# Kernel tuning notes

Measured on AMD Instinct MI355X. Metric: run time of the kernel, lower is better.

Reference implementation:

```python
import jax, jax.numpy as jnp
import numpy as np

WEIGHT = 1e-7
SIGMA_RGB = 15.0
SCALE = 0.5


def _nearest_resize(x, oh, ow):
    # PyTorch F.interpolate mode='nearest': src_idx = floor(dst * in/out)
    n, c, h, w = x.shape
    yi = (jnp.arange(oh) * (h / oh)).astype(jnp.int32)
    xi = (jnp.arange(ow) * (w / ow)).astype(jnp.int32)
    return x[:, :, yi][:, :, :, xi]


def _bilinear_resize(x, oh, ow):
    # PyTorch bilinear, align_corners=False: src = max((i+0.5)*in/out - 0.5, 0)
    n, k, h, w = x.shape

    def idx(o, s):
        src = jnp.maximum((jnp.arange(o, dtype=jnp.float32) + 0.5) * (s / o) - 0.5, 0.0)
        lo = jnp.floor(src).astype(jnp.int32)
        hi = jnp.minimum(lo + 1, s - 1)
        return lo, hi, src - lo

    ylo, yhi, fy = idx(oh, h)
    xlo, xhi, fx = idx(ow, w)
    top = x[:, :, ylo][:, :, :, xlo] * (1.0 - fx) + x[:, :, ylo][:, :, :, xhi] * fx
    bot = x[:, :, yhi][:, :, :, xlo] * (1.0 - fx) + x[:, :, yhi][:, :, :, xhi] * fx
    return top * (1.0 - fy)[:, None] + bot * fy[:, None]


def _bilateral_AS(feat, seg):
    # feat: [P,3] color features / sigma_rgb; seg: [K,P]
    # exact Gaussian color bilateral filter (what the permutohedral lattice approximates)
    sq = jnp.sum(feat * feat, axis=-1)                      # [P]
    d2 = sq[:, None] + sq[None, :] - 2.0 * (feat @ feat.T)  # [P,P]
    Kmat = jnp.exp(-0.5 * jnp.maximum(d2, 0.0))             # [P,P], symmetric
    return seg @ Kmat                                        # [K,P]


def setup_inputs() -> dict:
    key = jax.random.key(0)
    k1, k2 = jax.random.split(key)
    images = jax.random.uniform(k1, (4, 3, 128, 128), dtype=jnp.float32) * 255.0
    logits = jax.random.normal(k2, (4, 21, 128, 128), dtype=jnp.float32)
    segmentations = jax.nn.softmax(logits, axis=1)
    return {"images": images, "segmentations": segmentations}


def reference(images, segmentations):
    n, c, h, w = images.shape
    oh, ow = int(h * SCALE), int(w * SCALE)
    simg = _nearest_resize(images, oh, ow)            # [N,3,oh,ow]
    sseg = _bilinear_resize(segmentations, oh, ow)    # [N,K,oh,ow]
    P = oh * ow
    feats = simg.reshape(n, c, P).transpose(0, 2, 1) / SIGMA_RGB  # [N,P,3]
    segs = sseg.reshape(n, sseg.shape[1], P)                      # [N,K,P]
    AS = jax.vmap(_bilateral_AS)(feats, segs)                     # [N,K,P]
    loss = -jnp.sum(segs * AS) / jnp.float32(n)
    return (WEIGHT * loss).reshape(1)
```

## Files before the change

### kernel.cpp

```cpp
#include <hip/hip_runtime.h>


#define N_BATCH 4
#define IH 128
#define IW 128
#define P 4096
#define KC 21

using short8   = __attribute__((ext_vector_type(8))) short;
using floatx16 = __attribute__((ext_vector_type(16))) float;

static constexpr float INV_SIGMA = 1.0f / 15.0f;
static constexpr float LOG2E     = 1.4426950408889634f;
static constexpr float OUT_SCALE = -1e-7f / 4.0f;

#define ZP_OFF   0
#define ARGA_OFF 64
#define ARGB_OFF (ARGA_OFF + N_BATCH * P * 32)
#define SEG_OFF  (ARGB_OFF + N_BATCH * P * 32)
#define PART_OFF (SEG_OFF + N_BATCH * P * 48)

#define NFEAT (N_BATCH * P)
#define NSEG2 (N_BATCH * KC * P / 2)

#define CHUNKS 16
#define NBLOCKS (CHUNKS * 16 * N_BATCH)

__device__ __forceinline__ ushort f2bf(float x) {
    unsigned u = __builtin_bit_cast(unsigned, x);
    unsigned r = (u + 0x7FFFu + ((u >> 16) & 1u)) >> 16;
    return (ushort)r;
}
__device__ __forceinline__ float bf2f(ushort h) {
    return __builtin_bit_cast(float, (unsigned)h << 16);
}

__global__ void crf_prep(const float* __restrict__ img,
                         const float* __restrict__ seg,
                         char* __restrict__ wsb)
{
    int t = blockIdx.x * blockDim.x + threadIdx.x;
    if (t < NFEAT) {
        if (t < 16) ((float*)(wsb + ZP_OFF))[t] = 0.0f;

        int n = t >> 12;
        int p = t & (P - 1);
        int y = p >> 6, x = p & 63;

        const float* ib = img + (size_t)n * 3 * IH * IW + (size_t)(2 * y) * IW + 2 * x;
        float f0 = ib[0] * INV_SIGMA;
        float f1 = ib[IH * IW] * INV_SIGMA;
        float f2 = ib[2 * IH * IW] * INV_SIGMA;
        float h = 0.5f * (f0 * f0 + f1 * f1 + f2 * f2);

        float fa0 = f0 * LOG2E, fa1 = f1 * LOG2E, fa2 = f2 * LOG2E;
        ushort ah0 = f2bf(fa0), ah1 = f2bf(fa1), ah2 = f2bf(fa2);
        ushort al0 = f2bf(fa0 - bf2f(ah0));
        ushort al1 = f2bf(fa1 - bf2f(ah1));
        ushort al2 = f2bf(fa2 - bf2f(ah2));
        float nhL = -h * LOG2E;
        ushort nhh = f2bf(nhL), nhl = f2bf(nhL - bf2f(nhh));
        ushort bh0 = f2bf(f0), bh1 = f2bf(f1), bh2 = f2bf(f2);
        ushort bl0 = f2bf(f0 - bf2f(bh0));
        ushort bl1 = f2bf(f1 - bf2f(bh1));
        ushort bl2 = f2bf(f2 - bf2f(bh2));
        float hL = h * LOG2E;
        ushort hbh = f2bf(hL), hbl = f2bf(hL - bf2f(hbh));

        const ushort ONE = 0x3F80, NEG1 = 0xBF80;
        ushort rA[16] = {ah0, ah1, ah2, ah0, ah1, ah2, al0, al1, al2, al0, al1, al2,
                         nhh, nhl, NEG1, NEG1};
        ushort rB[16] = {bh0, bh1, bh2, bl0, bl1, bl2, bh0, bh1, bh2, bl0, bl1, bl2,
                         ONE, ONE, hbh, hbl};

        short8 vA0, vA1, vB0, vB1;
#pragma unroll
        for (int j = 0; j < 8; ++j) {
            vA0[j] = (short)rA[j];     vA1[j] = (short)rA[8 + j];
            vB0[j] = (short)rB[j];     vB1[j] = (short)rB[8 + j];
        }
        short8* dA = (short8*)(wsb + ARGA_OFF + (size_t)t * 32);
        dA[0] = vA0; dA[1] = vA1;
        short8* dB = (short8*)(wsb + ARGB_OFF + (size_t)t * 32);
        dB[0] = vB0; dB[1] = vB1;

        char* sp = wsb + SEG_OFF + (size_t)t * 48;
        *(ushort*)(sp + 42) = 0;
        *(uint*)(sp + 44) = 0;
    } else if (t < NFEAT + NSEG2) {
        int u = t - NFEAT;
        int pp = (u & 2047) * 2;
        int nk = u >> 11;
        int n = nk / 21;
        int k = nk - n * 21;
        int y = pp >> 6, x0 = pp & 63;

        const float* r0 = seg + (size_t)nk * IH * IW + (size_t)(2 * y) * IW + 2 * x0;
        float4 a = *(const float4*)r0;
        float4 b = *(const float4*)(r0 + IW);
        float v0 = 0.25f * ((a.x + a.y) + (b.x + b.y));
        float v1 = 0.25f * ((a.z + a.w) + (b.z + b.w));
        char* d = wsb + SEG_OFF + (size_t)(n * P + pp) * 48 + k * 2;
        *(ushort*)d = f2bf(v0);
        *(ushort*)(d + 48) = f2bf(v1);
    }
}

__global__ __launch_bounds__(256, 4) void crf_pair(char* __restrict__ wsb)
{
    const int n    = blockIdx.z;
    const int sp   = blockIdx.y;
    const int c    = blockIdx.x;
    const int wave = threadIdx.x >> 6;
    const int lane = threadIdx.x & 63;
    const int l32  = lane & 31;
    const int l5   = lane >> 5;

    const char* argA = wsb + ARGA_OFF + (size_t)n * P * 32;
    const char* argB = wsb + ARGB_OFF + (size_t)n * P * 32;
    const char* segT = wsb + SEG_OFF  + (size_t)n * P * 48;
    const char* zp   = wsb + ZP_OFF;

    const char* bBa = argB + l32 * 32 + l5 * 16;
    const char* bBs = segT + l32 * 48 + l5 * 16;
    const int maskH = l5 ? 0 : ~0;
    const char* bBh = l5 ? zp : (segT + l32 * 48 + 32);

    const floatx16 zc = {0.f,0.f,0.f,0.f,0.f,0.f,0.f,0.f,
                         0.f,0.f,0.f,0.f,0.f,0.f,0.f,0.f};

    short8 afA, afL, afH;

    float m0=0.f, m1=0.f, m2=0.f, m3=0.f;
    float d0=0.f, d1=0.f, d2=0.f, d3=0.f;

    auto jobM = [&](short8 ba, short8 bl, short8 bh) {
        floatx16 ar = __builtin_amdgcn_mfma_f32_32x32x16_bf16(afA, ba, zc, 0, 0, 0);
        floatx16 g  = __builtin_amdgcn_mfma_f32_32x32x16_bf16(afL, bl, zc, 0, 0, 0);
        g = __builtin_amdgcn_mfma_f32_32x32x16_bf16(afH, bh, g, 0, 0, 0);
#pragma unroll
        for (int r = 0; r < 16; ++r) {
            float t = __builtin_amdgcn_exp2f(ar[r]) * g[r];
            if ((r & 3) == 0) m0 += t;
            else if ((r & 3) == 1) m1 += t;
            else if ((r & 3) == 2) m2 += t;
            else m3 += t;
        }
    };
    auto jobD = [&](short8 ba, short8 bl, short8 bh) {
        floatx16 ar = __builtin_amdgcn_mfma_f32_32x32x16_bf16(afA, ba, zc, 0, 0, 0);
        floatx16 g  = __builtin_amdgcn_mfma_f32_32x32x16_bf16(afL, bl, zc, 0, 0, 0);
        g = __builtin_amdgcn_mfma_f32_32x32x16_bf16(afH, bh, g, 0, 0, 0);
#pragma unroll
        for (int r = 0; r < 16; ++r) {
            float t = __builtin_amdgcn_exp2f(ar[r]) * g[r];
            if ((r & 3) == 0) d0 += t;
            else if ((r & 3) == 1) d1 += t;
            else if ((r & 3) == 2) d2 += t;
            else d3 += t;
        }
    };

    auto load_A = [&](int ti) {
        int rr = ti * 32 + l32;
        afA = *(const short8*)(argA + rr * 32 + l5 * 16);
        afL = *(const short8*)(segT + rr * 48 + l5 * 16);
        afH = l5 ? *(const short8*)zp : *(const short8*)(segT + rr * 48 + 32);
    };

    auto run_main = [&](int jbase, int cnt) {
        if (cnt <= c) return;
        int nj = (cnt - c + CHUNKS - 1) / CHUNKS;
        int j0 = jbase + c;
        int oA0 = j0 * 1024, oS0 = j0 * 1536;
        int oA1 = oA0 + CHUNKS * 1024, oS1 = oS0 + CHUNKS * 1536;
        short8 a0 = *(const short8*)(bBa + oA0);
        short8 l0 = *(const short8*)(bBs + oS0);
        short8 h0 = *(const short8*)(bBh + (oS0 & maskH));
        short8 a1 = a0, l1 = l0, h1 = h0;
        if (nj > 1) {
            a1 = *(const short8*)(bBa + oA1);
            l1 = *(const short8*)(bBs + oS1);
            h1 = *(const short8*)(bBh + (oS1 & maskH));
        }
        for (int t = 0; t < nj; t += 2) {
            jobM(a0, l0, h0);
            if (t + 2 < nj) {
                oA0 += 2 * CHUNKS * 1024; oS0 += 2 * CHUNKS * 1536;
                a0 = *(const short8*)(bBa + oA0);
                l0 = *(const short8*)(bBs + oS0);
                h0 = *(const short8*)(bBh + (oS0 & maskH));
            }
            if (t + 1 < nj) {
                jobM(a1, l1, h1);
                if (t + 3 < nj) {
                    oA1 += 2 * CHUNKS * 1024; oS1 += 2 * CHUNKS * 1536;
                    a1 = *(const short8*)(bBa + oA1);
                    l1 = *(const short8*)(bBs + oS1);
                    h1 = *(const short8*)(bBh + (oS1 & maskH));
                }
            }
        }
    };

    auto run_edge = [&](int s) {
        for (int jj = wave; jj < 4; ++jj) {
            int j = 4 * s + jj;
            int oA = j * 1024, oS = j * 1536;
            short8 ba = *(const short8*)(bBa + oA);
            short8 bl = *(const short8*)(bBs + oS);
            short8 bh = *(const short8*)(bBh + (oS & maskH));
            if (jj == wave) jobD(ba, bl, bh);
            else           jobM(ba, bl, bh);
        }
    };

    const int s0 = sp, s1 = 31 - sp;

    load_A(4 * s0 + wave);
    run_main(4 * s0 + 4, 124 - 4 * sp);
    if (c == CHUNKS - 1) run_edge(s0);

    load_A(4 * s1 + wave);
    run_main(4 * s1 + 4, 4 * sp);
    if (c == CHUNKS - 2) run_edge(s1);

    float part = 2.0f * ((m0 + m1) + (m2 + m3)) + ((d0 + d1) + (d2 + d3));
#pragma unroll
    for (int off = 32; off > 0; off >>= 1)
        part += __shfl_down(part, off, 64);
    __shared__ float wsum[4];
    if (lane == 0) wsum[wave] = part;
    __syncthreads();
    if (threadIdx.x == 0) {
        int blin = (n * 16 + sp) * CHUNKS + c;
        ((float*)(wsb + PART_OFF))[blin] =
            (wsum[0] + wsum[1]) + (wsum[2] + wsum[3]);
    }
}

__global__ void crf_reduce(const char* __restrict__ wsb,
                           float* __restrict__ out)
{
    const float* part = (const float*)(wsb + PART_OFF);
    int t = threadIdx.x;
    float s = (part[t] + part[t + 256]) + (part[t + 512] + part[t + 768]);
#pragma unroll
    for (int off = 32; off > 0; off >>= 1)
        s += __shfl_down(s, off, 64);
    __shared__ float wsum[4];
    if ((t & 63) == 0) wsum[t >> 6] = s;
    __syncthreads();
    if (t == 0)
        out[0] = ((wsum[0] + wsum[1]) + (wsum[2] + wsum[3])) * OUT_SCALE;
}

extern "C" void kernel_launch(void* const* d_in, const int* in_sizes, int n_in,
                              void* d_out, int out_size, void* d_ws, size_t ws_size,
                              hipStream_t stream)
{
    const float* images = (const float*)d_in[0];
    const float* segm   = (const float*)d_in[1];
    float* out = (float*)d_out;
    char* wsb = (char*)d_ws;

    int prep_threads = NFEAT + NSEG2;
    crf_prep<<<dim3((prep_threads + 255) / 256), dim3(256), 0, stream>>>(
        images, segm, wsb);
    crf_pair<<<dim3(CHUNKS, 16, N_BATCH), dim3(256), 0, stream>>>(wsb);
    crf_reduce<<<dim3(1), dim3(256), 0, stream>>>(wsb, out);
}
```

Measured before the change: 70.83 us.

## Fuse final reduction into pair kernel via atomics and double chunk count

Drops the separate single-block reduce kernel. Each pair block now atomically adds its partial sum into one of 64 padded accumulators. A two-level atomic counter picks the last finishing block, which reads the accumulators, reduces them and writes the output. The grid is also split into twice as many chunks to raise parallelism. This saves one kernel launch and a dependency bubble, at the cost of atomic contention and relying on atomic ordering without an explicit fence.

```diff
diff --git a/kernel.cpp b/kernel.cpp
--- a/kernel.cpp
+++ b/kernel.cpp
@@ -18,12 +18,13 @@
 #define ARGA_OFF 64
 #define ARGB_OFF (ARGA_OFF + N_BATCH * P * 32)
 #define SEG_OFF  (ARGB_OFF + N_BATCH * P * 32)
-#define PART_OFF (SEG_OFF + N_BATCH * P * 48)
+#define ACC_OFF  (SEG_OFF + N_BATCH * P * 48)
+#define CNT_OFF  (ACC_OFF + 64 * 128)
 
 #define NFEAT (N_BATCH * P)
 #define NSEG2 (N_BATCH * KC * P / 2)
 
-#define CHUNKS 16
+#define CHUNKS 32
 #define NBLOCKS (CHUNKS * 16 * N_BATCH)
 
 __device__ __forceinline__ ushort f2bf(float x) {
@@ -42,6 +43,8 @@
     int t = blockIdx.x * blockDim.x + threadIdx.x;
     if (t < NFEAT) {
         if (t < 16) ((float*)(wsb + ZP_OFF))[t] = 0.0f;
+        else if (t < 80) ((float*)(wsb + ACC_OFF))[(t - 16) * 32] = 0.0f;
+        else if (t < 113) ((int*)(wsb + CNT_OFF))[(t - 80) * 32] = 0;
 
         int n = t >> 12;
         int p = t & (P - 1);
@@ -106,7 +109,8 @@
     }
 }
 
-__global__ __launch_bounds__(256, 4) void crf_pair(char* __restrict__ wsb)
+__global__ __launch_bounds__(256, 4) void crf_pair(char* __restrict__ wsb,
+                                                   float* __restrict__ out)
 {
     const int n    = blockIdx.z;
     const int sp   = blockIdx.y;
@@ -230,29 +234,31 @@
     for (int off = 32; off > 0; off >>= 1)
         part += __shfl_down(part, off, 64);
     __shared__ float wsum[4];
+    __shared__ int winner;
     if (lane == 0) wsum[wave] = part;
     __syncthreads();
+
+    float* acc = (float*)(wsb + ACC_OFF);
+    int*   cnt = (int*)(wsb + CNT_OFF);
     if (threadIdx.x == 0) {
+        float bsum = (wsum[0] + wsum[1]) + (wsum[2] + wsum[3]);
         int blin = (n * 16 + sp) * CHUNKS + c;
-        ((float*)(wsb + PART_OFF))[blin] =
-            (wsum[0] + wsum[1]) + (wsum[2] + wsum[3]);
+        float old = atomicAdd(&acc[(blin & 63) * 32], bsum);
+        asm volatile("" :: "v"(old));
+        int w = 0;
+        if (atomicAdd(&cnt[(blin >> 6) * 32], 1) == 63)
+            if (atomicAdd(&cnt[32 * 32], 1) == 31)
+                w = 1;
+        winner = w;
     }
-}
-
-__global__ void crf_reduce(const char* __restrict__ wsb,
-                           float* __restrict__ out)
-{
-    const float* part = (const float*)(wsb + PART_OFF);
-    int t = threadIdx.x;
-    float s = (part[t] + part[t + 256]) + (part[t + 512] + part[t + 768]);
-#pragma unroll
-    for (int off = 32; off > 0; off >>= 1)
-        s += __shfl_down(s, off, 64);
-    __shared__ float wsum[4];
-    if ((t & 63) == 0) wsum[t >> 6] = s;
     __syncthreads();
-    if (t == 0)
-        out[0] = ((wsum[0] + wsum[1]) + (wsum[2] + wsum[3])) * OUT_SCALE;
+    if (winner && threadIdx.x < 64) {
+        float v = atomicAdd(&acc[threadIdx.x * 32], 0.0f);
+#pragma unroll
+        for (int off = 32; off > 0; off >>= 1)
+            v += __shfl_down(v, off, 64);
+        if (threadIdx.x == 0) out[0] = v * OUT_SCALE;
+    }
 }
 
 extern "C" void kernel_launch(void* const* d_in, const int* in_sizes, int n_in,
@@ -267,6 +273,5 @@
     int prep_threads = NFEAT + NSEG2;
     crf_prep<<<dim3((prep_threads + 255) / 256), dim3(256), 0, stream>>>(
         images, segm, wsb);
-    crf_pair<<<dim3(CHUNKS, 16, N_BATCH), dim3(256), 0, stream>>>(wsb);
-    crf_reduce<<<dim3(1), dim3(256), 0, stream>>>(wsb, out);
-}
+    crf_pair<<<dim3(CHUNKS, 16, N_BATCH), dim3(256), 0, stream>>>(wsb, out);
+}
```

After: 73.57 us. 3.9% more time.
